# Performance work log

Measured on AMD Instinct MI355X. Metric: run time of the kernel, lower is better.

The kernel has to match this reference:

```python
import jax, jax.numpy as jnp
import numpy as np

N_NODES = 20000
N_EDGES = 320000
N_GRAPHS = 512
N_FEAT = 29
DIMS = [N_FEAT, 1024, 512, 256, 512, 1024]
EPS = 1e-5


def setup_inputs() -> dict:
    key = jax.random.key(0)
    ks = jax.random.split(key, 32)
    inp = {}
    inp["x"] = jax.random.normal(ks[0], (N_NODES, N_FEAT), dtype=jnp.float32)
    inp["edge_index"] = jax.random.randint(ks[1], (2, N_EDGES), 0, N_NODES, dtype=jnp.int64)
    inp["batch"] = jnp.sort(jax.random.randint(ks[2], (N_NODES,), 0, N_GRAPHS, dtype=jnp.int64))
    # 5 GCNConv layers: weight [in, out] + bias, plus BN gamma/beta
    for i in range(5):
        din, dout = DIMS[i], DIMS[i + 1]
        inp[f"W{i+1}"] = jax.random.normal(ks[3 + i], (din, dout), dtype=jnp.float32) * (1.0 / np.sqrt(din))
        inp[f"b{i+1}"] = jnp.zeros((dout,), dtype=jnp.float32)
        inp[f"g{i+1}"] = jnp.ones((dout,), dtype=jnp.float32)
        inp[f"be{i+1}"] = jnp.zeros((dout,), dtype=jnp.float32)
    # attention gate Linear(1024, 1)
    inp["Wg"] = jax.random.normal(ks[10], (1024, 1), dtype=jnp.float32) * 0.03
    inp["bg"] = jnp.zeros((1,), dtype=jnp.float32)
    # MLP head
    inp["Wf2"] = jax.random.normal(ks[11], (1024, 128), dtype=jnp.float32) * 0.03
    inp["bf2"] = jnp.zeros((128,), dtype=jnp.float32)
    inp["Wf3"] = jax.random.normal(ks[12], (128, 16), dtype=jnp.float32) * 0.25
    inp["bf3"] = jnp.zeros((16,), dtype=jnp.float32)
    inp["Wf4"] = jax.random.normal(ks[13], (16, 1), dtype=jnp.float32) * 0.25
    inp["bf4"] = jnp.zeros((1,), dtype=jnp.float32)
    return inp


def _gcn_conv(x, row, col, W, b):
    # PyG GCNConv: linear transform, then D^{-1/2}(A+I)D^{-1/2} aggregation, then bias.
    n = x.shape[0]
    xw = x @ W  # [N, dout]
    deg = jax.ops.segment_sum(jnp.ones_like(col, dtype=xw.dtype), col, num_segments=n)
    dinv = jnp.where(deg > 0, jax.lax.rsqrt(deg), 0.0)
    norm = dinv[row] * dinv[col]  # [E+N]
    out = jax.ops.segment_sum(xw[row] * norm[:, None], col, num_segments=n)
    return out + b


def _bn_train(x, gamma, beta):
    m = jnp.mean(x, axis=0)
    v = jnp.var(x, axis=0)  # biased, matches torch training normalization
    return gamma * (x - m) * jax.lax.rsqrt(v + EPS) + beta


def _global_attention(x, batch, Wg, bg, n_graphs):
    gate = (x @ Wg + bg)[:, 0]  # [N]
    gmax = jax.ops.segment_max(gate, batch, num_segments=n_graphs)
    e = jnp.exp(gate - gmax[batch])
    s = jax.ops.segment_sum(e, batch, num_segments=n_graphs)
    alpha = e / s[batch]
    return jax.ops.segment_sum(alpha[:, None] * x, batch, num_segments=n_graphs)


def reference(x, edge_index, batch,
              W1, b1, g1, be1, W2, b2, g2, be2, W3, b3, g3, be3,
              W4, b4, g4, be4, W5, b5, g5, be5,
              Wg, bg, Wf2, bf2, Wf3, bf3, Wf4, bf4):
    n = x.shape[0]
    sl = jnp.arange(n, dtype=edge_index.dtype)
    row = jnp.concatenate([edge_index[0], sl])  # with self-loops
    col = jnp.concatenate([edge_index[1], sl])
    h = x
    params = [(W1, b1, g1, be1), (W2, b2, g2, be2), (W3, b3, g3, be3),
              (W4, b4, g4, be4), (W5, b5, g5, be5)]
    for (W, b, g, be) in params:
        h = jax.nn.relu(_gcn_conv(h, row, col, W, b))
        h = _bn_train(h, g, be)
    p = _global_attention(h, batch, Wg, bg, N_GRAPHS)  # [G, 1024]
    p = jax.nn.relu(p @ Wf2 + bf2)
    p = jax.nn.relu(p @ Wf3 + bf3)
    return p @ Wf4 + bf4  # [G, 1]
```

## Files before the change

kernel.cpp:

```cpp
#include <hip/hip_runtime.h>

#define EPS_BN 1e-5f

constexpr int NN   = 20000;
constexpr int NE   = 320000;
constexpr int NTOT = NE + NN;
constexpr int NG   = 512;
constexpr int MPAD = 20480;
constexpr int NBLK = 79;

typedef _Float16 half8  __attribute__((ext_vector_type(8)));
typedef _Float16 half2v __attribute__((ext_vector_type(2)));
typedef float floatx4   __attribute__((ext_vector_type(4)));

__device__ __forceinline__ void gload_lds16(const void* g, void* l) {
  __builtin_amdgcn_global_load_lds(
      (const __attribute__((address_space(1))) void*)g,
      (__attribute__((address_space(3))) void*)l, 16, 0, 0);
}

__global__ void k_deg(const int* __restrict__ col, int* __restrict__ deg,
                      const int* __restrict__ batch, int* __restrict__ gcnt) {
  int e = blockIdx.x * blockDim.x + threadIdx.x;
  if (e >= NTOT) return;
  int c = (e < NE) ? col[e] : (e - NE);
  atomicAdd(&deg[c], 1);
  if (e < NN) atomicAdd(&gcnt[batch[e]], 1);
}

__global__ __launch_bounds__(256) void k_pre1(const int* __restrict__ deg,
                                              float* __restrict__ dinvv,
                                              int* __restrict__ psum) {
  __shared__ int ws[4];
  int t = threadIdx.x, lane = t & 63, wv = t >> 6;
  int idx = blockIdx.x * 256 + t;
  int d = (idx < NN) ? deg[idx] : 0;
  if (idx < NN) dinvv[idx] = rsqrtf((float)d);
  int s = d;
  for (int o = 1; o < 64; o <<= 1) { int u = __shfl_up(s, o, 64); if (lane >= o) s += u; }
  if (lane == 63) ws[wv] = s;
  __syncthreads();
  if (t == 0) psum[blockIdx.x] = ws[0] + ws[1] + ws[2] + ws[3];
}

__global__ __launch_bounds__(256) void k_pre2(const int* __restrict__ psum,
                                              int* __restrict__ pbase,
                                              const int* __restrict__ gcnt,
                                              int* __restrict__ goff) {
  __shared__ int ws[8];
  int t = threadIdx.x, lane = t & 63, wv = t >> 6;
  int v = (t < NBLK) ? psum[t] : 0;
  int inc = v;
  for (int o = 1; o < 64; o <<= 1) { int u = __shfl_up(inc, o, 64); if (lane >= o) inc += u; }
  if (lane == 63) ws[wv] = inc;
  __syncthreads();
  int base = 0;
  for (int w = 0; w < wv; ++w) base += ws[w];
  int excl = base + inc - v;
  if (t < NBLK) pbase[t] = excl;
  if (t == NBLK - 1) pbase[NBLK] = excl + v;
  __syncthreads();
  int a0 = gcnt[2 * t], a1 = gcnt[2 * t + 1];
  int p = a0 + a1;
  int incp = p;
  for (int o = 1; o < 64; o <<= 1) { int u = __shfl_up(incp, o, 64); if (lane >= o) incp += u; }
  if (lane == 63) ws[4 + wv] = incp;
  __syncthreads();
  int gb = 0;
  for (int w = 0; w < wv; ++w) gb += ws[4 + w];
  int exclp = gb + incp - p;
  goff[2 * t]     = exclp;
  goff[2 * t + 1] = exclp + a0;
  if (t == 255) goff[NG] = exclp + p;
}

__global__ __launch_bounds__(256) void k_pre3(const int* __restrict__ deg,
                                              const int* __restrict__ pbase,
                                              int* __restrict__ indptr,
                                              int* __restrict__ cursor) {
  __shared__ int ws[4];
  int t = threadIdx.x, lane = t & 63, wv = t >> 6;
  int idx = blockIdx.x * 256 + t;
  int d = (idx < NN) ? deg[idx] : 0;
  int inc = d;
  for (int o = 1; o < 64; o <<= 1) { int u = __shfl_up(inc, o, 64); if (lane >= o) inc += u; }
  if (lane == 63) ws[wv] = inc;
  __syncthreads();
  int base = pbase[blockIdx.x];
  for (int w = 0; w < wv; ++w) base += ws[w];
  int excl = base + inc - d;
  if (idx < NN) { indptr[idx] = excl; cursor[idx] = excl; }
  if (idx == NN - 1) indptr[NN] = excl + d;
}

__global__ void k_fill(const int* __restrict__ row, const int* __restrict__ col,
                       const float* __restrict__ dinv, int* __restrict__ cursor,
                       int2* __restrict__ csw, float* __restrict__ rsum) {
  int e = blockIdx.x * blockDim.x + threadIdx.x;
  if (e >= NTOT) return;
  int r, c;
  if (e < NE) { r = row[e]; c = col[e]; } else { r = c = e - NE; }
  float wv = dinv[r] * dinv[c];
  int pos = atomicAdd(&cursor[c], 1);
  int2 m; m.x = r; m.y = __builtin_bit_cast(int, wv);
  csw[pos] = m;
  atomicAdd(&rsum[c], wv);
}

__device__ __forceinline__ size_t fragoff(int n, int k, int kb) {
  return ((size_t)(n >> 4) * kb + (k >> 5)) * 512 + ((k >> 3) & 3) * 128 + (n & 15) * 8;
}

__global__ void k_wconv3(const float* __restrict__ W0, const float* __restrict__ W3,
                         const float* __restrict__ W4,
                         _Float16* __restrict__ T0, _Float16* __restrict__ T3,
                         _Float16* __restrict__ T4) {
  int c = blockIdx.x * blockDim.x + threadIdx.x;
  _Float16 ov[8];
  if (c < 4096) {
    int n = c >> 2, k = (c & 3) * 8;
    #pragma unroll
    for (int i = 0; i < 8; ++i)
      ov[i] = (_Float16)((k + i < 29) ? W0[(size_t)(k + i) * 1024 + n] : 0.f);
    *(uint4*)&T0[fragoff(n, k, 1)] = *(const uint4*)ov;
  } else if (c < 4096 + 16384) {
    int c2 = c - 4096;
    int n = c2 >> 5, k = (c2 & 31) * 8;
    #pragma unroll
    for (int i = 0; i < 8; ++i)
      ov[i] = (_Float16)W3[(size_t)(k + i) * 512 + n];
    *(uint4*)&T3[fragoff(n, k, 8)] = *(const uint4*)ov;
  } else if (c < 4096 + 16384 + 65536) {
    int c3 = c - 20480;
    int n = c3 >> 6, k = (c3 & 63) * 8;
    #pragma unroll
    for (int i = 0; i < 8; ++i)
      ov[i] = (_Float16)W4[(size_t)(k + i) * 1024 + n];
    *(uint4*)&T4[fragoff(n, k, 16)] = *(const uint4*)ov;
  }
}

__global__ __launch_bounds__(256) void k_wfold(const float* __restrict__ W, int K, int N,
                                               const float* __restrict__ sums,
                                               const float* __restrict__ gamma,
                                               const float* __restrict__ beta,
                                               _Float16* __restrict__ T,
                                               float* __restrict__ c) {
  __shared__ float red[256];
  int n = blockIdx.x, tid = threadIdx.x;
  int kb = K >> 5;
  const float inv_n = 1.f / NN;
  float csum = 0.f;
  for (int kc = tid; kc < (K >> 3); kc += 256) {
    int k = kc * 8;
    _Float16 ov[8];
    #pragma unroll
    for (int i = 0; i < 8; ++i) {
      int ki = k + i;
      float mean = sums[ki] * inv_n;
      float var  = sums[K + ki] * inv_n - mean * mean;
      float sc   = gamma[ki] * rsqrtf(var + EPS_BN);
      float sh   = beta[ki] - mean * sc;
      float wv   = W[(size_t)ki * N + n];
      ov[i] = (_Float16)(sc * wv);
      csum += sh * wv;
    }
    *(uint4*)&T[fragoff(n, k, kb)] = *(const uint4*)ov;
  }
  red[tid] = csum;
  __syncthreads();
  for (int o = 128; o > 0; o >>= 1) {
    if (tid < o) red[tid] += red[tid + o];
    __syncthreads();
  }
  if (tid == 0) c[n] = red[0];
}

#define AGG_CH 128
__global__ __launch_bounds__(128) void k_agg29(
    const float* __restrict__ X,
    const int* __restrict__ indptr, const int2* __restrict__ csw,
    _Float16* __restrict__ Y) {
  __shared__ int   s_src[AGG_CH];
  __shared__ float s_w[AGG_CH];
  __shared__ float red[128];
  int node = blockIdx.x;
  int tid  = threadIdx.x;
  int sub  = tid / 29;
  int feat = tid - sub * 29;
  bool act = tid < 116;
  int beg = indptr[node], end = indptr[node + 1];
  float acc = 0.f;
  for (int e0 = beg; e0 < end; e0 += AGG_CH) {
    int c = min(AGG_CH, end - e0);
    if (tid < c) {
      int2 m = csw[e0 + tid];
      s_src[tid] = m.x;
      s_w[tid]   = __builtin_bit_cast(float, m.y);
    }
    __syncthreads();
    if (act) {
      for (int j = 0; j < c; j += 4) {
        int jj = j + sub;
        if (jj < c) acc += s_w[jj] * X[(size_t)s_src[jj] * 29 + feat];
      }
    }
    __syncthreads();
  }
  red[tid] = acc;
  __syncthreads();
  if (tid < 32) {
    float v = 0.f;
    if (tid < 29) v = red[tid] + red[29 + tid] + red[58 + tid] + red[87 + tid];
    Y[(size_t)node * 32 + tid] = (_Float16)v;
  }
}

template<int MODE>
__global__ __launch_bounds__(256) void k_aggv(
    const _Float16* __restrict__ X, _Float16* __restrict__ Y,
    const int* __restrict__ indptr, const int2* __restrict__ csw,
    const float* __restrict__ rowsum,
    const float* __restrict__ p0, const float* __restrict__ p1,
    const float* __restrict__ p2)
{
  constexpr int F = 512;
  int wave = threadIdx.x >> 6;
  int lane = threadIdx.x & 63;
  int node = blockIdx.x * 4 + wave;
  int beg = indptr[node], end = indptr[node + 1];
  float acc[8];
  #pragma unroll
  for (int i = 0; i < 8; ++i) acc[i] = 0.f;
  const unsigned* Xl = (const unsigned*)X + lane * 4;

  auto body = [&](int e) {
    int2 m = csw[e];
    float we = __builtin_bit_cast(float, m.y);
    uint4 d = *(const uint4*)(Xl + (size_t)m.x * (F / 2));
    unsigned uu[4] = {d.x, d.y, d.z, d.w};
    #pragma unroll
    for (int i = 0; i < 4; ++i) {
      half2v h = __builtin_bit_cast(half2v, uu[i]);
      acc[2 * i]     = fmaf(we, (float)h[0], acc[2 * i]);
      acc[2 * i + 1] = fmaf(we, (float)h[1], acc[2 * i + 1]);
    }
  };
  int e = beg;
  for (; e + 8 <= end; e += 8) {
    body(e); body(e + 1); body(e + 2); body(e + 3);
    body(e + 4); body(e + 5); body(e + 6); body(e + 7);
  }
  for (; e < end; ++e) body(e);

  float s_n = rowsum[node];
  size_t ob = (size_t)node * F + lane * 8;
  _Float16 outv[8];
  #pragma unroll
  for (int i = 0; i < 8; ++i) {
    int f = lane * 8 + i;
    float v;
    if constexpr (MODE == 0) {
      v = fmaxf(acc[i] + s_n * p0[f] + p1[f], 0.f);
    } else {
      const float inv_n = 1.f / NN;
      float mean = p0[f] * inv_n;
      float var  = p0[F + f] * inv_n - mean * mean;
      float sc   = p1[f] * rsqrtf(var + EPS_BN);
      float sh   = p2[f] - mean * sc;
      v = sc * acc[i] + s_n * sh;
    }
    outv[i] = (_Float16)v;
  }
  *(uint4*)(Y + ob) = *(const uint4*)outv;
}

template<int MODE>
__global__ __launch_bounds__(256) void k_aggp(
    const _Float16* __restrict__ X, _Float16* __restrict__ Y,
    const int* __restrict__ indptr, const int2* __restrict__ csw,
    const float* __restrict__ rowsum,
    const float* __restrict__ p0, const float* __restrict__ p1,
    const float* __restrict__ p2)
{
  constexpr int F = 256;
  int wave = threadIdx.x >> 6;
  int lane = threadIdx.x & 63;
  int half = lane >> 5;
  int l32  = lane & 31;
  int node = blockIdx.x * 8 + wave * 2 + half;
  int beg = indptr[node], end = indptr[node + 1];
  int len = end - beg;
  int len0 = __shfl(len, 0, 64);
  int len1 = __shfl(len, 32, 64);
  int maxlen = max(len0, len1);

  float acc[8];
  #pragma unroll
  for (int i = 0; i < 8; ++i) acc[i] = 0.f;
  const unsigned* Xl = (const unsigned*)X + l32 * 4;

  auto body = [&](int t) {
    int e = beg + min(t, len - 1);
    int2 m = csw[e];
    float we = (t < len) ? __builtin_bit_cast(float, m.y) : 0.f;
    uint4 d = *(const uint4*)(Xl + (size_t)m.x * (F / 2));
    unsigned uu[4] = {d.x, d.y, d.z, d.w};
    #pragma unroll
    for (int i = 0; i < 4; ++i) {
      half2v h = __builtin_bit_cast(half2v, uu[i]);
      acc[2 * i]     = fmaf(we, (float)h[0], acc[2 * i]);
      acc[2 * i + 1] = fmaf(we, (float)h[1], acc[2 * i + 1]);
    }
  };
  int t = 0;
  for (; t + 4 <= maxlen; t += 4) { body(t); body(t + 1); body(t + 2); body(t + 3); }
  for (; t < maxlen; ++t) body(t);

  float s_n = rowsum[node];
  size_t ob = (size_t)node * F + l32 * 8;
  _Float16 outv[8];
  #pragma unroll
  for (int i = 0; i < 8; ++i) {
    int f = l32 * 8 + i;
    float v;
    if constexpr (MODE == 0) {
      v = fmaxf(acc[i] + s_n * p0[f] + p1[f], 0.f);
    } else {
      const float inv_n = 1.f / NN;
      float mean = p0[f] * inv_n;
      float var  = p0[F + f] * inv_n - mean * mean;
      float sc   = p1[f] * rsqrtf(var + EPS_BN);
      float sh   = p2[f] - mean * sc;
      v = sc * acc[i] + s_n * sh;
    }
    outv[i] = (_Float16)v;
  }
  *(uint4*)(Y + ob) = *(const uint4*)outv;
}

template<int BK>
__global__ __launch_bounds__(256) void k_gemm16(
    const _Float16* __restrict__ A, const _Float16* __restrict__ Bf,
    const float* __restrict__ bias,
    _Float16* __restrict__ Ch,
    float* __restrict__ stats,
    int N, int K, int do_relu, int nbx)
{
  __shared__ __align__(16) union UU {
    _Float16 a[128 * BK];
    _Float16 c[128 * 136];
  } u;
  __shared__ float sred[256];

  const int tid  = threadIdx.x;
  const int wave = tid >> 6;
  const int lane = tid & 63;

  int lin = blockIdx.x;
  int xcd = lin & 7, seq = lin >> 3;
  int bx = seq % nbx, grp = seq / nbx;
  int by = xcd + 8 * grp;
  const int row0 = by * 128;
  const int col0 = bx * 128;

  const int q  = lane >> 4;
  const int mm = lane & 15;
  const int wm = wave >> 1;
  const int wn = wave & 1;

  sred[tid] = 0.f;

  constexpr int NREP = (BK == 32) ? 2 : 4;
  constexpr int RPW  = (BK == 32) ? 16 : 8;
  const _Float16* pA[NREP];
  _Float16* dstA[NREP];
  {
    int rl = (BK == 32) ? (lane >> 2) : (lane >> 3);
    int cp = (BK == 32) ? (lane & 3) : (lane & 7);
    #pragma unroll
    for (int rep = 0; rep < NREP; ++rep) {
      int trow = wave * 32 + rep * RPW;
      int s = (BK == 32) ? ((lane >> 3) & 3) : ((rep & 1) * 4 + (rl >> 1));
      int csrc = cp ^ s;
      pA[rep] = A + (size_t)(row0 + trow + rl) * K + csrc * 8;
      dstA[rep] = u.a + trow * BK;
    }
  }

  const int sR = (BK == 32) ? ((mm >> 1) & 3) : (mm >> 1);
  int rdA[4];
  #pragma unroll
  for (int i = 0; i < 4; ++i) rdA[i] = (wm * 64 + i * 16 + mm) * BK;

  const int kb = K >> 5;
  const _Float16* pb[4];
  #pragma unroll
  for (int j = 0; j < 4; ++j)
    pb[j] = Bf + (size_t)((col0 + wn * 64 + j * 16) >> 4) * kb * 512 + lane * 8;

  floatx4 acc[4][4];
  #pragma unroll
  for (int i = 0; i < 4; ++i)
    #pragma unroll
    for (int j = 0; j < 4; ++j) acc[i][j] = floatx4{0.f, 0.f, 0.f, 0.f};

  for (int k0 = 0; k0 < K; k0 += BK) {
    #pragma unroll
    for (int rep = 0; rep < NREP; ++rep) {
      gload_lds16(pA[rep], dstA[rep]);
      pA[rep] += BK;
    }
    __syncthreads();

    #pragma unroll
    for (int kk = 0; kk < BK / 32; ++kk) {
      half8 bv[4];
      #pragma unroll
      for (int j = 0; j < 4; ++j) { bv[j] = *(const half8*)pb[j]; pb[j] += 512; }
      int pos = ((q + 4 * kk) ^ sR) * 8;
      half8 av[4];
      #pragma unroll
      for (int i = 0; i < 4; ++i) av[i] = *(const half8*)&u.a[rdA[i] + pos];
      #pragma unroll
      for (int j = 0; j < 4; ++j)
        #pragma unroll
        for (int i = 0; i < 4; ++i)
          acc[i][j] = __builtin_amdgcn_mfma_f32_16x16x32_f16(av[i], bv[j], acc[i][j], 0, 0, 0);
    }
    __syncthreads();
  }

  float sloc[4]  = {0.f, 0.f, 0.f, 0.f};
  float s2loc[4] = {0.f, 0.f, 0.f, 0.f};
  #pragma unroll
  for (int j = 0; j < 4; ++j) {
    int cl = wn * 64 + j * 16 + mm;
    float bv = bias ? bias[col0 + cl] : 0.f;
    #pragma unroll
    for (int i = 0; i < 4; ++i) {
      #pragma unroll
      for (int r = 0; r < 4; ++r) {
        int rl = wm * 64 + i * 16 + q * 4 + r;
        float v = acc[i][j][r] + bv;
        if (do_relu) v = fmaxf(v, 0.f);
        u.c[rl * 136 + cl] = (_Float16)v;
        if (row0 + rl < NN) { sloc[j] += v; s2loc[j] += v * v; }
      }
    }
  }

  if (stats) {
    #pragma unroll
    for (int j = 0; j < 4; ++j) {
      float a = sloc[j], b2 = s2loc[j];
      a  += __shfl_xor(a, 16, 64);  a  += __shfl_xor(a, 32, 64);
      b2 += __shfl_xor(b2, 16, 64); b2 += __shfl_xor(b2, 32, 64);
      if (q == 0) {
        int cl = wn * 64 + j * 16 + mm;
        atomicAdd(&sred[cl], a);
        atomicAdd(&sred[128 + cl], b2);
      }
    }
  }
  __syncthreads();

  #pragma unroll
  for (int pass = 0; pass < 8; ++pass) {
    int cidx = tid + pass * 256;
    int r = cidx >> 4, kc = cidx & 15;
    int rr = row0 + r;
    if (rr < NN) {
      uint4 d = *(const uint4*)&u.c[r * 136 + kc * 8];
      *(uint4*)&Ch[(size_t)rr * N + col0 + kc * 8] = d;
    }
  }

  if (stats && tid < 128) {
    atomicAdd(&stats[col0 + tid], sred[tid]);
    atomicAdd(&stats[N + col0 + tid], sred[128 + tid]);
  }
}

__global__ __launch_bounds__(256) void k_stats16(const _Float16* __restrict__ X, int F,
                                                 float* __restrict__ sums) {
  int tid = threadIdx.x;
  int npf = F >> 8;
  float s[2] = {0.f, 0.f}, s2[2] = {0.f, 0.f};
  for (int r = blockIdx.x; r < NN; r += gridDim.x) {
    #pragma unroll
    for (int i = 0; i < 2; ++i) {
      if (i < npf) {
        float v = (float)X[(size_t)r * F + tid + i * 256];
        s[i] += v; s2[i] += v * v;
      }
    }
  }
  #pragma unroll
  for (int i = 0; i < 2; ++i) {
    if (i < npf) {
      atomicAdd(&sums[tid + i * 256], s[i]);
      atomicAdd(&sums[F + tid + i * 256], s2[i]);
    }
  }
}

__global__ __launch_bounds__(256) void k_gate2(const _Float16* __restrict__ X,
                                               const float* __restrict__ sums,
                                               const float* __restrict__ g5,
                                               const float* __restrict__ be5,
                                               const float* __restrict__ Wg,
                                               const float* __restrict__ bg,
                                               float* __restrict__ gate) {
  __shared__ float red[512];
  int n = blockIdx.x, tid = threadIdx.x;
  int f = tid * 4;
  const float inv_n = 1.f / NN;
  uint2 u = *(const uint2*)(X + (size_t)n * 1024 + f);
  half2v h0 = __builtin_bit_cast(half2v, u.x);
  half2v h1 = __builtin_bit_cast(half2v, u.y);
  float xv[4] = {(float)h0[0], (float)h0[1], (float)h1[0], (float)h1[1]};
  float s = 0.f, t = 0.f;
  #pragma unroll
  for (int i = 0; i < 4; ++i) {
    int ff = f + i;
    float mean = sums[ff] * inv_n;
    float var  = sums[1024 + ff] * inv_n - mean * mean;
    float sc   = g5[ff] * rsqrtf(var + EPS_BN);
    float sh   = be5[ff] - mean * sc;
    float wg   = Wg[ff];
    s += xv[i] * (sc * wg);
    t += sh * wg;
  }
  red[tid] = s;
  red[256 + tid] = t;
  __syncthreads();
  for (int o = 128; o > 0; o >>= 1) {
    if (tid < o) { red[tid] += red[tid + o]; red[256 + tid] += red[256 + tid + o]; }
    __syncthreads();
  }
  if (tid == 0) gate[n] = red[0] + red[256] + bg[0];
}

__global__ __launch_bounds__(256) void k_poolhead(
    const _Float16* __restrict__ X, const float* __restrict__ gate,
    const int* __restrict__ goff,
    const float* __restrict__ sums, const float* __restrict__ g5,
    const float* __restrict__ be5,
    const float* __restrict__ Wf2, const float* __restrict__ bf2,
    const float* __restrict__ Wf3, const float* __restrict__ bf3,
    const float* __restrict__ Wf4, const float* __restrict__ bf4,
    float* __restrict__ out)
{
  __shared__ float red[256];
  __shared__ float sp[1024];
  __shared__ float sp2[128];
  __shared__ float sp3[16];
  int g = blockIdx.x, tid = threadIdx.x;
  int beg = goff[g], end = goff[g + 1];
  bool nonempty = end > beg;

  float m = -3.4e38f;
  for (int n = beg + tid; n < end; n += 256) m = fmaxf(m, gate[n]);
  red[tid] = m;
  __syncthreads();
  for (int o = 128; o > 0; o >>= 1) {
    if (tid < o) red[tid] = fmaxf(red[tid], red[tid + o]);
    __syncthreads();
  }
  m = red[0];
  __syncthreads();
  float s = 0.f;
  for (int n = beg + tid; n < end; n += 256) s += expf(gate[n] - m);
  red[tid] = s;
  __syncthreads();
  for (int o = 128; o > 0; o >>= 1) {
    if (tid < o) red[tid] += red[tid + o];
    __syncthreads();
  }
  float inv = nonempty ? (1.f / red[0]) : 0.f;

  int f = tid * 4;
  const float inv_n = 1.f / NN;
  float acc[4] = {0.f, 0.f, 0.f, 0.f};
  if (nonempty) {
    const _Float16* Xf = X + f;
    int n = beg;
    for (; n + 4 <= end; n += 4) {
      float a0 = expf(gate[n]     - m);
      float a1 = expf(gate[n + 1] - m);
      float a2 = expf(gate[n + 2] - m);
      float a3 = expf(gate[n + 3] - m);
      uint2 u0 = *(const uint2*)(Xf + (size_t)(n)     * 1024);
      uint2 u1 = *(const uint2*)(Xf + (size_t)(n + 1) * 1024);
      uint2 u2 = *(const uint2*)(Xf + (size_t)(n + 2) * 1024);
      uint2 u3 = *(const uint2*)(Xf + (size_t)(n + 3) * 1024);
      half2v p00 = __builtin_bit_cast(half2v, u0.x), p01 = __builtin_bit_cast(half2v, u0.y);
      half2v p10 = __builtin_bit_cast(half2v, u1.x), p11 = __builtin_bit_cast(half2v, u1.y);
      half2v p20 = __builtin_bit_cast(half2v, u2.x), p21 = __builtin_bit_cast(half2v, u2.y);
      half2v p30 = __builtin_bit_cast(half2v, u3.x), p31 = __builtin_bit_cast(half2v, u3.y);
      acc[0] += a0 * (float)p00[0] + a1 * (float)p10[0] + a2 * (float)p20[0] + a3 * (float)p30[0];
      acc[1] += a0 * (float)p00[1] + a1 * (float)p10[1] + a2 * (float)p20[1] + a3 * (float)p30[1];
      acc[2] += a0 * (float)p01[0] + a1 * (float)p11[0] + a2 * (float)p21[0] + a3 * (float)p31[0];
      acc[3] += a0 * (float)p01[1] + a1 * (float)p11[1] + a2 * (float)p21[1] + a3 * (float)p31[1];
    }
    for (; n < end; ++n) {
      float a = expf(gate[n] - m);
      uint2 u0 = *(const uint2*)(Xf + (size_t)n * 1024);
      half2v p0 = __builtin_bit_cast(half2v, u0.x), p1 = __builtin_bit_cast(half2v, u0.y);
      acc[0] += a * (float)p0[0];
      acc[1] += a * (float)p0[1];
      acc[2] += a * (float)p1[0];
      acc[3] += a * (float)p1[1];
    }
  }
  #pragma unroll
  for (int i = 0; i < 4; ++i) {
    int ff = f + i;
    float mean = sums[ff] * inv_n;
    float var  = sums[1024 + ff] * inv_n - mean * mean;
    float sc   = g5[ff] * rsqrtf(var + EPS_BN);
    float sh   = be5[ff] - mean * sc;
    sp[ff] = nonempty ? (acc[i] * inv * sc + sh) : 0.f;
  }
  __syncthreads();

  if (tid < 128) {
    float s2 = bf2[tid];
    for (int k = 0; k < 1024; ++k) s2 += sp[k] * Wf2[k * 128 + tid];
    sp2[tid] = fmaxf(s2, 0.f);
  }
  __syncthreads();
  if (tid < 16) {
    float t = bf3[tid];
    for (int k = 0; k < 128; ++k) t += sp2[k] * Wf3[k * 16 + tid];
    sp3[tid] = fmaxf(t, 0.f);
  }
  __syncthreads();
  if (tid == 0) {
    float t = bf4[0];
    for (int k = 0; k < 16; ++k) t += sp3[k] * Wf4[k];
    out[g] = t;
  }
}

extern "C" void kernel_launch(void* const* d_in, const int* in_sizes, int n_in,
                              void* d_out, int out_size, void* d_ws, size_t ws_size,
                              hipStream_t stream) {
  const float* x     = (const float*)d_in[0];
  const int*   ei    = (const int*)d_in[1];
  const int*   batch = (const int*)d_in[2];
  const float* W[5]; const float* b[5]; const float* g[5]; const float* be[5];
  for (int l = 0; l < 5; ++l) {
    W[l]  = (const float*)d_in[3 + 4 * l];
    b[l]  = (const float*)d_in[4 + 4 * l];
    g[l]  = (const float*)d_in[5 + 4 * l];
    be[l] = (const float*)d_in[6 + 4 * l];
  }
  const float* Wg  = (const float*)d_in[23];
  const float* bg  = (const float*)d_in[24];
  const float* Wf2 = (const float*)d_in[25];
  const float* bf2 = (const float*)d_in[26];
  const float* Wf3 = (const float*)d_in[27];
  const float* bf3 = (const float*)d_in[28];
  const float* Wf4 = (const float*)d_in[29];
  const float* bf4 = (const float*)d_in[30];
  float* out = (float*)d_out;

  const int* row = ei;
  const int* col = ei + NE;

  char* base = (char*)d_ws;
  size_t off = 0;
  auto alloc = [&](size_t bytes) -> char* {
    char* p = base + off;
    off = (off + bytes + 255) & ~(size_t)255;
    return p;
  };
  _Float16*  AH  = (_Float16*)alloc((size_t)MPAD * 1024 * 2);
  _Float16*  ASM = (_Float16*)alloc((size_t)MPAD * 32 * 2);
  _Float16*  BF  = (_Float16*)alloc((size_t)NN * 512 * 2);
  _Float16*  BF2 = (_Float16*)alloc((size_t)NN * 512 * 2);
  _Float16*  H5  = (_Float16*)alloc((size_t)NN * 1024 * 2);
  const int wtsz[5] = {1024 * 32, 512 * 1024, 256 * 512, 512 * 256, 1024 * 512};
  _Float16* WT[5];
  for (int l = 0; l < 5; ++l) WT[l] = (_Float16*)alloc((size_t)wtsz[l] * 2);
  float* c2  = (float*)alloc(512 * 4);
  float* c3  = (float*)alloc(256 * 4);
  float* dinv    = (float*)alloc(NN * 4);
  int*   indptr  = (int*)alloc((NN + 1) * 4);
  int*   cursor  = (int*)alloc(NN * 4);
  int2*  csw     = (int2*)alloc((size_t)NTOT * 8);
  int*   psum    = (int*)alloc((NBLK + 1) * 4);
  int*   pbase   = (int*)alloc((NBLK + 1) * 4);
  int*   goff    = (int*)alloc((NG + 1) * 4);
  float* gate    = (float*)alloc(NN * 4);
  size_t znf = 6656 + NN + NG + NN;
  float* zbase = (float*)alloc(znf * 4);
  float* bns  = zbase;
  int*   deg  = (int*)(zbase + 6656);
  int*   gcnt = (int*)(zbase + 6656 + NN);
  float* rsum = zbase + 6656 + NN + NG;
  float* bns1 = bns;
  float* bns2 = bns + 2048;
  float* bns3 = bns + 3072;
  float* bns4 = bns + 3584;
  float* bns5 = bns + 4608;

  hipMemsetAsync(zbase, 0, znf * 4, stream);
  k_deg<<<(NTOT + 255) / 256, 256, 0, stream>>>(col, deg, batch, gcnt);
  k_pre1<<<NBLK, 256, 0, stream>>>(deg, dinv, psum);
  k_pre2<<<1, 256, 0, stream>>>(psum, pbase, gcnt, goff);
  k_pre3<<<NBLK, 256, 0, stream>>>(deg, pbase, indptr, cursor);
  k_fill<<<(NTOT + 255) / 256, 256, 0, stream>>>(row, col, dinv, cursor, csw, rsum);
  k_wconv3<<<336, 256, 0, stream>>>(W[0], W[3], W[4], WT[0], WT[3], WT[4]);

  auto gemm = [&](const _Float16* Aop, int wl, const float* bias,
                  _Float16* Ch, float* stats, int Nn, int Kk, int relu) {
    int nbx = Nn / 128;
    if (Kk == 32)
      k_gemm16<32><<<nbx * 160, 256, 0, stream>>>(Aop, WT[wl], bias, Ch, stats, Nn, Kk, relu, nbx);
    else
      k_gemm16<64><<<nbx * 160, 256, 0, stream>>>(Aop, WT[wl], bias, Ch, stats, Nn, Kk, relu, nbx);
  };

  k_agg29<<<NN, 128, 0, stream>>>(x, indptr, csw, ASM);
  gemm(ASM, 0, b[0], AH, bns1, 1024, 32, 1);

  k_wfold<<<512, 256, 0, stream>>>(W[1], 1024, 512, bns1, g[0], be[0], WT[1], c2);
  gemm(AH, 1, nullptr, BF, nullptr, 512, 1024, 0);
  k_aggv<0><<<NN / 4, 256, 0, stream>>>(BF, AH, indptr, csw, rsum, c2, b[1], nullptr);
  k_stats16<<<512, 256, 0, stream>>>(AH, 512, bns2);

  k_wfold<<<256, 256, 0, stream>>>(W[2], 512, 256, bns2, g[1], be[1], WT[2], c3);
  gemm(AH, 2, nullptr, BF2, nullptr, 256, 512, 0);
  k_aggp<0><<<NN / 8, 256, 0, stream>>>(BF2, BF, indptr, csw, rsum, c3, b[2], nullptr);
  k_stats16<<<512, 256, 0, stream>>>(BF, 256, bns3);

  k_aggp<1><<<NN / 8, 256, 0, stream>>>(BF, AH, indptr, csw, rsum, bns3, g[2], be[2]);
  gemm(AH, 3, b[3], BF2, bns4, 512, 256, 1);

  k_aggv<1><<<NN / 4, 256, 0, stream>>>(BF2, AH, indptr, csw, rsum, bns4, g[3], be[3]);
  gemm(AH, 4, b[4], H5, bns5, 1024, 512, 1);

  k_gate2<<<NN, 256, 0, stream>>>(H5, bns5, g[4], be[4], Wg, bg, gate);
  k_poolhead<<<NG, 256, 0, stream>>>(H5, gate, goff, bns5, g[4], be[4],
                                     Wf2, bf2, Wf3, bf3, Wf4, bf4, out);
}
```

Baseline: 590.3 us.

## Store GEMM A operands in MFMA fragment layout and load directly to registers

Producers (agg29, aggv, aggp, and the first GEMM epilogue) now write activations in a pre-tiled 16-row by 32-k fragment layout. The GEMM then reads A fragments straight from global memory into registers with a one-step software prefetch, instead of staging A through LDS with barriers. This removes the LDS traffic and the per-k-step syncthreads, at the cost of an extra fragment-layout buffer, dual writes in some aggregation kernels, and loss of LDS-level reuse of A across waves. Some kernels still write the row layout because the stats kernels need it.

Measured after the change: 603.6 us. +2.2%, slower.

```diff
diff --git a/kernel.cpp b/kernel.cpp
--- a/kernel.cpp
+++ b/kernel.cpp
@@ -12,12 +12,6 @@
 typedef _Float16 half8  __attribute__((ext_vector_type(8)));
 typedef _Float16 half2v __attribute__((ext_vector_type(2)));
 typedef float floatx4   __attribute__((ext_vector_type(4)));
-
-__device__ __forceinline__ void gload_lds16(const void* g, void* l) {
-  __builtin_amdgcn_global_load_lds(
-      (const __attribute__((address_space(1))) void*)g,
-      (__attribute__((address_space(3))) void*)l, 16, 0, 0);
-}
 
 __global__ void k_deg(const int* __restrict__ col, int* __restrict__ deg,
                       const int* __restrict__ batch, int* __restrict__ gcnt) {
@@ -212,13 +206,15 @@
   if (tid < 32) {
     float v = 0.f;
     if (tid < 29) v = red[tid] + red[29 + tid] + red[58 + tid] + red[87 + tid];
-    Y[(size_t)node * 32 + tid] = (_Float16)v;
+    size_t fb = (size_t)(node >> 4) * 512 + (size_t)(tid >> 3) * 128 + (node & 15) * 8 + (tid & 7);
+    Y[fb] = (_Float16)v;
   }
 }
 
 template<int MODE>
 __global__ __launch_bounds__(256) void k_aggv(
-    const _Float16* __restrict__ X, _Float16* __restrict__ Y,
+    const _Float16* __restrict__ X,
+    _Float16* __restrict__ Yf, _Float16* __restrict__ Yrow,
     const int* __restrict__ indptr, const int2* __restrict__ csw,
     const float* __restrict__ rowsum,
     const float* __restrict__ p0, const float* __restrict__ p1,
@@ -254,7 +250,6 @@
   for (; e < end; ++e) body(e);
 
   float s_n = rowsum[node];
-  size_t ob = (size_t)node * F + lane * 8;
   _Float16 outv[8];
   #pragma unroll
   for (int i = 0; i < 8; ++i) {
@@ -272,12 +267,19 @@
     }
     outv[i] = (_Float16)v;
   }
-  *(uint4*)(Y + ob) = *(const uint4*)outv;
+  if (Yf) {
+    size_t fb = (size_t)(node >> 4) * (16 * 512) + lane * 128 + (node & 15) * 8;
+    *(uint4*)(Yf + fb) = *(const uint4*)outv;
+  }
+  if (Yrow) {
+    *(uint4*)(Yrow + (size_t)node * F + lane * 8) = *(const uint4*)outv;
+  }
 }
 
 template<int MODE>
 __global__ __launch_bounds__(256) void k_aggp(
-    const _Float16* __restrict__ X, _Float16* __restrict__ Y,
+    const _Float16* __restrict__ X,
+    _Float16* __restrict__ Yf, _Float16* __restrict__ Yrow,
     const int* __restrict__ indptr, const int2* __restrict__ csw,
     const float* __restrict__ rowsum,
     const float* __restrict__ p0, const float* __restrict__ p1,
@@ -318,7 +320,6 @@
   for (; t < maxlen; ++t) body(t);
 
   float s_n = rowsum[node];
-  size_t ob = (size_t)node * F + l32 * 8;
   _Float16 outv[8];
   #pragma unroll
   for (int i = 0; i < 8; ++i) {
@@ -336,21 +337,25 @@
     }
     outv[i] = (_Float16)v;
   }
-  *(uint4*)(Y + ob) = *(const uint4*)outv;
-}
-
-template<int BK>
-__global__ __launch_bounds__(256) void k_gemm16(
-    const _Float16* __restrict__ A, const _Float16* __restrict__ Bf,
+  if (Yf) {
+    size_t fb = (size_t)(node >> 4) * (8 * 512) + l32 * 128 + (node & 15) * 8;
+    *(uint4*)(Yf + fb) = *(const uint4*)outv;
+  }
+  if (Yrow) {
+    *(uint4*)(Yrow + (size_t)node * F + l32 * 8) = *(const uint4*)outv;
+  }
+}
+
+template<int K, int FRAGOUT>
+__global__ __launch_bounds__(256) void k_gemmf(
+    const _Float16* __restrict__ Af, const _Float16* __restrict__ Bf,
     const float* __restrict__ bias,
     _Float16* __restrict__ Ch,
+    _Float16* __restrict__ Cf,
     float* __restrict__ stats,
-    int N, int K, int do_relu, int nbx)
+    int N, int do_relu, int nbx)
 {
-  __shared__ __align__(16) union UU {
-    _Float16 a[128 * BK];
-    _Float16 c[128 * 136];
-  } u;
+  __shared__ __align__(16) _Float16 cs[128 * 136];
   __shared__ float sred[256];
 
   const int tid  = threadIdx.x;
@@ -371,33 +376,15 @@
 
   sred[tid] = 0.f;
 
-  constexpr int NREP = (BK == 32) ? 2 : 4;
-  constexpr int RPW  = (BK == 32) ? 16 : 8;
-  const _Float16* pA[NREP];
-  _Float16* dstA[NREP];
-  {
-    int rl = (BK == 32) ? (lane >> 2) : (lane >> 3);
-    int cp = (BK == 32) ? (lane & 3) : (lane & 7);
-    #pragma unroll
-    for (int rep = 0; rep < NREP; ++rep) {
-      int trow = wave * 32 + rep * RPW;
-      int s = (BK == 32) ? ((lane >> 3) & 3) : ((rep & 1) * 4 + (rl >> 1));
-      int csrc = cp ^ s;
-      pA[rep] = A + (size_t)(row0 + trow + rl) * K + csrc * 8;
-      dstA[rep] = u.a + trow * BK;
-    }
-  }
-
-  const int sR = (BK == 32) ? ((mm >> 1) & 3) : (mm >> 1);
-  int rdA[4];
-  #pragma unroll
-  for (int i = 0; i < 4; ++i) rdA[i] = (wm * 64 + i * 16 + mm) * BK;
-
-  const int kb = K >> 5;
+  constexpr int KB = K / 32;
+  const _Float16* pa[4];
   const _Float16* pb[4];
   #pragma unroll
+  for (int i = 0; i < 4; ++i)
+    pa[i] = Af + (size_t)((row0 >> 4) + wm * 4 + i) * (KB * 512) + lane * 8;
+  #pragma unroll
   for (int j = 0; j < 4; ++j)
-    pb[j] = Bf + (size_t)((col0 + wn * 64 + j * 16) >> 4) * kb * 512 + lane * 8;
+    pb[j] = Bf + (size_t)((col0 >> 4) + wn * 4 + j) * (KB * 512) + lane * 8;
 
   floatx4 acc[4][4];
   #pragma unroll
@@ -405,46 +392,50 @@
     #pragma unroll
     for (int j = 0; j < 4; ++j) acc[i][j] = floatx4{0.f, 0.f, 0.f, 0.f};
 
-  for (int k0 = 0; k0 < K; k0 += BK) {
-    #pragma unroll
-    for (int rep = 0; rep < NREP; ++rep) {
-      gload_lds16(pA[rep], dstA[rep]);
-      pA[rep] += BK;
-    }
-    __syncthreads();
-
-    #pragma unroll
-    for (int kk = 0; kk < BK / 32; ++kk) {
-      half8 bv[4];
+  half8 av[4], bv[4];
+  #pragma unroll
+  for (int i = 0; i < 4; ++i) { av[i] = *(const half8*)pa[i]; pa[i] += 512; }
+  #pragma unroll
+  for (int j = 0; j < 4; ++j) { bv[j] = *(const half8*)pb[j]; pb[j] += 512; }
+
+  #pragma unroll 2
+  for (int s = 0; s < KB; ++s) {
+    half8 nav[4], nbv[4];
+    if (s + 1 < KB) {
       #pragma unroll
-      for (int j = 0; j < 4; ++j) { bv[j] = *(const half8*)pb[j]; pb[j] += 512; }
-      int pos = ((q + 4 * kk) ^ sR) * 8;
-      half8 av[4];
+      for (int i = 0; i < 4; ++i) { nav[i] = *(const half8*)pa[i]; pa[i] += 512; }
       #pragma unroll
-      for (int i = 0; i < 4; ++i) av[i] = *(const half8*)&u.a[rdA[i] + pos];
+      for (int j = 0; j < 4; ++j) { nbv[j] = *(const half8*)pb[j]; pb[j] += 512; }
+    }
+    #pragma unroll
+    for (int j = 0; j < 4; ++j)
       #pragma unroll
-      for (int j = 0; j < 4; ++j)
-        #pragma unroll
-        for (int i = 0; i < 4; ++i)
-          acc[i][j] = __builtin_amdgcn_mfma_f32_16x16x32_f16(av[i], bv[j], acc[i][j], 0, 0, 0);
-    }
-    __syncthreads();
-  }
+      for (int i = 0; i < 4; ++i)
+        acc[i][j] = __builtin_amdgcn_mfma_f32_16x16x32_f16(av[i], bv[j], acc[i][j], 0, 0, 0);
+    if (s + 1 < KB) {
+      #pragma unroll
+      for (int i = 0; i < 4; ++i) av[i] = nav[i];
+      #pragma unroll
+      for (int j = 0; j < 4; ++j) bv[j] = nbv[j];
+    }
+  }
+
+  __syncthreads();
 
   float sloc[4]  = {0.f, 0.f, 0.f, 0.f};
   float s2loc[4] = {0.f, 0.f, 0.f, 0.f};
   #pragma unroll
   for (int j = 0; j < 4; ++j) {
     int cl = wn * 64 + j * 16 + mm;
-    float bv = bias ? bias[col0 + cl] : 0.f;
+    float bvv = bias ? bias[col0 + cl] : 0.f;
     #pragma unroll
     for (int i = 0; i < 4; ++i) {
       #pragma unroll
       for (int r = 0; r < 4; ++r) {
         int rl = wm * 64 + i * 16 + q * 4 + r;
-        float v = acc[i][j][r] + bv;
+        float v = acc[i][j][r] + bvv;
         if (do_relu) v = fmaxf(v, 0.f);
-        u.c[rl * 136 + cl] = (_Float16)v;
+        cs[rl * 136 + cl] = (_Float16)v;
         if (row0 + rl < NN) { sloc[j] += v; s2loc[j] += v * v; }
       }
     }
@@ -465,14 +456,28 @@
   }
   __syncthreads();
 
-  #pragma unroll
-  for (int pass = 0; pass < 8; ++pass) {
-    int cidx = tid + pass * 256;
-    int r = cidx >> 4, kc = cidx & 15;
-    int rr = row0 + r;
-    if (rr < NN) {
-      uint4 d = *(const uint4*)&u.c[r * 136 + kc * 8];
-      *(uint4*)&Ch[(size_t)rr * N + col0 + kc * 8] = d;
+  if (FRAGOUT) {
+    int mlo = tid & 15, sub = (tid >> 4) & 3, kcr = (tid >> 6) & 3;
+    int kbN = N >> 5;
+    #pragma unroll
+    for (int pass = 0; pass < 8; ++pass) {
+      int m = pass * 16 + mlo;
+      int kl = kcr * 32 + sub * 8;
+      uint4 d = *(const uint4*)&cs[m * 136 + kl];
+      size_t fa = ((size_t)((row0 >> 4) + pass) * kbN + (col0 >> 5) + kcr) * 512
+                + sub * 128 + mlo * 8;
+      *(uint4*)&Cf[fa] = d;
+    }
+  } else {
+    #pragma unroll
+    for (int pass = 0; pass < 8; ++pass) {
+      int cidx = tid + pass * 256;
+      int r = cidx >> 4, kc = cidx & 15;
+      int rr = row0 + r;
+      if (rr < NN) {
+        uint4 d = *(const uint4*)&cs[r * 136 + kc * 8];
+        *(uint4*)&Ch[(size_t)rr * N + col0 + kc * 8] = d;
+      }
     }
   }
 
@@ -678,6 +683,7 @@
     return p;
   };
   _Float16*  AH  = (_Float16*)alloc((size_t)MPAD * 1024 * 2);
+  _Float16*  AF  = (_Float16*)alloc((size_t)MPAD * 512 * 2);
   _Float16*  ASM = (_Float16*)alloc((size_t)MPAD * 32 * 2);
   _Float16*  BF  = (_Float16*)alloc((size_t)NN * 512 * 2);
   _Float16*  BF2 = (_Float16*)alloc((size_t)NN * 512 * 2);
@@ -715,33 +721,24 @@
   k_fill<<<(NTOT + 255) / 256, 256, 0, stream>>>(row, col, dinv, cursor, csw, rsum);
   k_wconv3<<<336, 256, 0, stream>>>(W[0], W[3], W[4], WT[0], WT[3], WT[4]);
 
-  auto gemm = [&](const _Float16* Aop, int wl, const float* bias,
-                  _Float16* Ch, float* stats, int Nn, int Kk, int relu) {
-    int nbx = Nn / 128;
-    if (Kk == 32)
-      k_gemm16<32><<<nbx * 160, 256, 0, stream>>>(Aop, WT[wl], bias, Ch, stats, Nn, Kk, relu, nbx);
-    else
-      k_gemm16<64><<<nbx * 160, 256, 0, stream>>>(Aop, WT[wl], bias, Ch, stats, Nn, Kk, relu, nbx);
-  };
-
   k_agg29<<<NN, 128, 0, stream>>>(x, indptr, csw, ASM);
-  gemm(ASM, 0, b[0], AH, bns1, 1024, 32, 1);
+  k_gemmf<32, 1><<<8 * 160, 256, 0, stream>>>(ASM, WT[0], b[0], nullptr, AH, bns1, 1024, 1, 8);
 
   k_wfold<<<512, 256, 0, stream>>>(W[1], 1024, 512, bns1, g[0], be[0], WT[1], c2);
-  gemm(AH, 1, nullptr, BF, nullptr, 512, 1024, 0);
-  k_aggv<0><<<NN / 4, 256, 0, stream>>>(BF, AH, indptr, csw, rsum, c2, b[1], nullptr);
+  k_gemmf<1024, 0><<<4 * 160, 256, 0, stream>>>(AH, WT[1], nullptr, BF, nullptr, nullptr, 512, 0, 4);
+  k_aggv<0><<<NN / 4, 256, 0, stream>>>(BF, AF, AH, indptr, csw, rsum, c2, b[1], nullptr);
   k_stats16<<<512, 256, 0, stream>>>(AH, 512, bns2);
 
   k_wfold<<<256, 256, 0, stream>>>(W[2], 512, 256, bns2, g[1], be[1], WT[2], c3);
-  gemm(AH, 2, nullptr, BF2, nullptr, 256, 512, 0);
-  k_aggp<0><<<NN / 8, 256, 0, stream>>>(BF2, BF, indptr, csw, rsum, c3, b[2], nullptr);
+  k_gemmf<512, 0><<<2 * 160, 256, 0, stream>>>(AF, WT[2], nullptr, BF2, nullptr, nullptr, 256, 0, 2);
+  k_aggp<0><<<NN / 8, 256, 0, stream>>>(BF2, nullptr, BF, indptr, csw, rsum, c3, b[2], nullptr);
   k_stats16<<<512, 256, 0, stream>>>(BF, 256, bns3);
 
-  k_aggp<1><<<NN / 8, 256, 0, stream>>>(BF, AH, indptr, csw, rsum, bns3, g[2], be[2]);
-  gemm(AH, 3, b[3], BF2, bns4, 512, 256, 1);
-
-  k_aggv<1><<<NN / 4, 256, 0, stream>>>(BF2, AH, indptr, csw, rsum, bns4, g[3], be[3]);
-  gemm(AH, 4, b[4], H5, bns5, 1024, 512, 1);
+  k_aggp<1><<<NN / 8, 256, 0, stream>>>(BF, AH, nullptr, indptr, csw, rsum, bns3, g[2], be[2]);
+  k_gemmf<256, 0><<<4 * 160, 256, 0, stream>>>(AH, WT[3], b[3], BF2, nullptr, bns4, 512, 1, 4);
+
+  k_aggv<1><<<NN / 4, 256, 0, stream>>>(BF2, AF, nullptr, indptr, csw, rsum, bns4, g[3], be[3]);
+  k_gemmf<512, 0><<<8 * 160, 256, 0, stream>>>(AF, WT[4], b[4], H5, nullptr, bns5, 1024, 1, 8);
 
   k_gate2<<<NN, 256, 0, stream>>>(H5, bns5, g[4], be[4], Wg, bg, gate);
   k_poolhead<<<NG, 256, 0, stream>>>(H5, gate, goff, bns5, g[4], be[4],
```
